# Optimization experiments

Measured on AMD Instinct MI355X. Metric: run time of the kernel, lower is better.

## Reference

```python
import jax, jax.numpy as jnp
import numpy as np

B, R, N, D, H = 32, 5, 1024, 256, 256

def setup_inputs() -> dict:
    key = jax.random.key(0)
    k1, k2, k3, k4 = jax.random.split(key, 4)
    nodes = jax.random.normal(k1, (B, N, D), dtype=jnp.float32)
    adj = jax.random.uniform(k2, (B, R, N, N), dtype=jnp.float32)
    # kaiming_normal_ approximation: std = sqrt(2 / fan_in)
    std = np.sqrt(2.0 / D).astype(np.float32)
    w_0 = jax.random.normal(k3, (H, D), dtype=jnp.float32) * std
    w_r = jax.random.normal(k4, (R, H, D), dtype=jnp.float32) * std
    return {"nodes": nodes, "adj": adj, "w_0": w_0, "w_r": w_r}

def reference(nodes, adj, w_0, w_r):
    # nodes: (B,N,D), adj: (B,R,N,N), w_0: (H,D), w_r: (R,H,D)
    xw_0 = jnp.einsum('bnd,hd->bnh', nodes, w_0)            # (B,N,H)
    xw_r = jnp.einsum('bnd,rhd->brnh', nodes, w_r)          # (B,R,N,H)
    c_r = jnp.sum(adj, axis=-1, keepdims=True)              # (B,R,N,1)
    c_r = jnp.where(c_r == 0, jnp.ones_like(c_r), c_r)
    out = jnp.sum(xw_r / c_r, axis=1) + xw_0                # (B,N,H)
    # dropout is identity in eval mode
    return out
```

## Files before the change

### kernel.cpp

```cpp
#include <hip/hip_runtime.h>
#include <hip/hip_bf16.h>


#define BB 32
#define RR 5
#define NN 1024
#define DD 256
#define HH 256
#define MM (BB * NN)

typedef __attribute__((ext_vector_type(8))) short short8;
typedef __attribute__((ext_vector_type(4))) float f32x4;

#define GAS(p) ((const __attribute__((address_space(1))) void*)(p))
#define LAS(p) ((__attribute__((address_space(3))) void*)(p))

__device__ __forceinline__ unsigned short f2bf(float f) {
    unsigned int u = __float_as_uint(f);
    unsigned int r = (u + 0x7FFFu + ((u >> 16) & 1u)) >> 16;
    return (unsigned short)r;
}

__global__ void cvt_kernel(const float* __restrict__ in,
                           unsigned short* __restrict__ out, int n) {
    int i = (blockIdx.x * blockDim.x + threadIdx.x) * 4;
    if (i >= n) return;
    float4 v = *reinterpret_cast<const float4*>(in + i);
    ushort4 o;
    o.x = f2bf(v.x); o.y = f2bf(v.y); o.z = f2bf(v.z); o.w = f2bf(v.w);
    *reinterpret_cast<ushort4*>(out + i) = o;
}

__global__ __launch_bounds__(256) void rowsum_kernel(const float* __restrict__ adj,
                                                     float* __restrict__ inv_c) {
    const int wave = blockIdx.x * 4 + (threadIdx.x >> 6);
    const int lane = threadIdx.x & 63;
    const float4* row4 = reinterpret_cast<const float4*>(adj + (size_t)wave * NN);
    float s = 0.f;
#pragma unroll
    for (int i = 0; i < 4; ++i) {
        float4 v = row4[lane + 64 * i];
        s += (v.x + v.y) + (v.z + v.w);
    }
#pragma unroll
    for (int off = 32; off > 0; off >>= 1) s += __shfl_down(s, off, 64);
    if (lane == 0) {
        float c = (s == 0.f) ? 1.f : s;
        inv_c[wave] = 1.f / c;
    }
}

__global__ __launch_bounds__(256) void gemm_kernel(
    const unsigned short* __restrict__ nodesb,
    const unsigned short* __restrict__ wb,
    const float* __restrict__ inv_c,
    float* __restrict__ out) {
    __shared__ unsigned short smem[14336];
    __shared__ float s_inv[RR * 64];

    const int tid  = threadIdx.x;
    const int lane = tid & 63;
    const int wv   = tid >> 6;
    const int row_base = blockIdx.x * 64;
    const int col_base = blockIdx.y * 64;
    const int m    = lane & 15;
    const int quad = lane >> 4;

    const unsigned short* gp[7];
    unsigned short*       lp[7];
#pragma unroll
    for (int j = 0; j < 7; ++j) {
        const int c = wv * 7 + j;
        lp[j] = smem + c * 512;
        if (c < 4) {
            const int u   = c * 64 + lane;
            const int row = u >> 2;
            const int kc  = u & 3;
            gp[j] = nodesb + (size_t)(row_base + row) * DD + kc * 8;
        } else {
            const int u    = (c - 4) * 64 + lane;
            const int col6 = u >> 2;
            const int kc   = u & 3;
            const int set  = col6 >> 6;
            const int col  = col6 & 63;
            gp[j] = wb + (size_t)(set * HH + col_base + col) * DD + kc * 8;
        }
    }

    f32x4 acc[6][4];
#pragma unroll
    for (int s = 0; s < 6; ++s)
#pragma unroll
        for (int t = 0; t < 4; ++t) acc[s][t] = (f32x4){0.f, 0.f, 0.f, 0.f};

    const unsigned short* aL = smem + m * 32 + quad * 8;
    const unsigned short* bL = smem + 2048 + (wv * 16 + m) * 32 + quad * 8;

    for (int kt = 0; kt < 8; ++kt) {
        __syncthreads();
#pragma unroll
        for (int j = 0; j < 7; ++j)
            __builtin_amdgcn_global_load_lds(GAS(gp[j] + kt * 32), LAS(lp[j]), 16, 0, 0);
        __syncthreads();

        short8 afr[4];
#pragma unroll
        for (int t = 0; t < 4; ++t)
            afr[t] = *reinterpret_cast<const short8*>(aL + t * 512);
#pragma unroll
        for (int s = 0; s < 6; ++s) {
            short8 bfr = *reinterpret_cast<const short8*>(bL + s * 2048);
#pragma unroll
            for (int t = 0; t < 4; ++t)
                acc[s][t] = __builtin_amdgcn_mfma_f32_16x16x32_bf16(afr[t], bfr, acc[s][t], 0, 0, 0);
        }
    }

    const int b  = row_base >> 10;
    const int n0 = row_base & (NN - 1);
    __syncthreads();
#pragma unroll
    for (int i = tid; i < RR * 64; i += 256) {
        const int r = i >> 6, nl = i & 63;
        s_inv[i] = inv_c[((size_t)b * RR + r) * NN + n0 + nl];
    }
    __syncthreads();

    const int hcol = col_base + wv * 16 + m;
#pragma unroll
    for (int t = 0; t < 4; ++t) {
#pragma unroll
        for (int i = 0; i < 4; ++i) {
            const int rloc = t * 16 + quad * 4 + i;
            float v = acc[0][t][i];
#pragma unroll
            for (int r = 0; r < RR; ++r)
                v += s_inv[r * 64 + rloc] * acc[r + 1][t][i];
            out[(size_t)(row_base + rloc) * HH + hcol] = v;
        }
    }
}

extern "C" void kernel_launch(void* const* d_in, const int* in_sizes, int n_in,
                              void* d_out, int out_size, void* d_ws, size_t ws_size,
                              hipStream_t stream) {
    const float* nodes = (const float*)d_in[0];
    const float* adj   = (const float*)d_in[1];
    const float* w0    = (const float*)d_in[2];
    const float* wr    = (const float*)d_in[3];
    float* out = (float*)d_out;

    unsigned short* nodesb = (unsigned short*)d_ws;
    unsigned short* wb     = (unsigned short*)((char*)d_ws + (size_t)MM * DD * 2);
    float*          inv_c  = (float*)((char*)d_ws + (size_t)MM * DD * 2 + (size_t)6 * HH * DD * 2);

    const int n_nodes = MM * DD;
    const int n_w0    = HH * DD;
    const int n_wr    = RR * HH * DD;

    cvt_kernel<<<n_nodes / 4 / 256, 256, 0, stream>>>(nodes, nodesb, n_nodes);
    cvt_kernel<<<n_w0 / 4 / 256, 256, 0, stream>>>(w0, wb, n_w0);
    cvt_kernel<<<n_wr / 4 / 256, 256, 0, stream>>>(wr, wb + n_w0, n_wr);

    rowsum_kernel<<<(BB * RR * NN) / 4, 256, 0, stream>>>(adj, inv_c);

    gemm_kernel<<<dim3(MM / 64, HH / 64), 256, 0, stream>>>(nodesb, wb, inv_c, out);
}
```

Before: 906.4 us.

## Fuse conversion and rowsum kernels; double-buffer GEMM LDS loads

Merges the three bf16 conversion launches and the adjacency row-sum into one prep kernel, so there are fewer launches and the conversion traffic overlaps the adj streaming. The GEMM gets a two-stage LDS ring buffer filled by async global-to-LDS loads, synchronised with vmcnt waits and raw barriers, so loads for tile k+2 overlap compute on tile k. This doubles LDS use per block, which may lower occupancy, and relies on hand-written waitcnt accounting being correct.

```diff
diff --git a/kernel.cpp b/kernel.cpp
--- a/kernel.cpp
+++ b/kernel.cpp
@@ -21,20 +21,33 @@
     return (unsigned short)r;
 }
 
-__global__ void cvt_kernel(const float* __restrict__ in,
-                           unsigned short* __restrict__ out, int n) {
-    int i = (blockIdx.x * blockDim.x + threadIdx.x) * 4;
-    if (i >= n) return;
-    float4 v = *reinterpret_cast<const float4*>(in + i);
-    ushort4 o;
-    o.x = f2bf(v.x); o.y = f2bf(v.y); o.z = f2bf(v.z); o.w = f2bf(v.w);
-    *reinterpret_cast<ushort4*>(out + i) = o;
-}
+__global__ __launch_bounds__(256) void prep_kernel(
+    const float* __restrict__ adj, float* __restrict__ inv_c,
+    const float* __restrict__ nodes, unsigned short* __restrict__ nodesb,
+    const float* __restrict__ w0, const float* __restrict__ wr,
+    unsigned short* __restrict__ wb) {
+    const int tid  = threadIdx.x;
+    const int lane = tid & 63;
 
-__global__ __launch_bounds__(256) void rowsum_kernel(const float* __restrict__ adj,
-                                                     float* __restrict__ inv_c) {
-    const int wave = blockIdx.x * 4 + (threadIdx.x >> 6);
-    const int lane = threadIdx.x & 63;
+    const int gid = blockIdx.x * 256 + tid;
+    const int i4  = gid * 4;
+    if (i4 < MM * DD) {
+        float4 v = *reinterpret_cast<const float4*>(nodes + i4);
+        ushort4 o;
+        o.x = f2bf(v.x); o.y = f2bf(v.y); o.z = f2bf(v.z); o.w = f2bf(v.w);
+        *reinterpret_cast<ushort4*>(nodesb + i4) = o;
+    }
+    if (gid < (HH * DD + RR * HH * DD) / 4) {
+        const int i = gid * 4;
+        float4 v;
+        if (i < HH * DD) v = *reinterpret_cast<const float4*>(w0 + i);
+        else             v = *reinterpret_cast<const float4*>(wr + (i - HH * DD));
+        ushort4 o;
+        o.x = f2bf(v.x); o.y = f2bf(v.y); o.z = f2bf(v.z); o.w = f2bf(v.w);
+        *reinterpret_cast<ushort4*>(wb + i) = o;
+    }
+
+    const int wave = blockIdx.x * 4 + (tid >> 6);
     const float4* row4 = reinterpret_cast<const float4*>(adj + (size_t)wave * NN);
     float s = 0.f;
 #pragma unroll
@@ -55,7 +68,7 @@
     const unsigned short* __restrict__ wb,
     const float* __restrict__ inv_c,
     float* __restrict__ out) {
-    __shared__ unsigned short smem[14336];
+    __shared__ unsigned short smem[2 * 14336];
     __shared__ float s_inv[RR * 64];
 
     const int tid  = threadIdx.x;
@@ -93,26 +106,41 @@
 #pragma unroll
         for (int t = 0; t < 4; ++t) acc[s][t] = (f32x4){0.f, 0.f, 0.f, 0.f};
 
-    const unsigned short* aL = smem + m * 32 + quad * 8;
-    const unsigned short* bL = smem + 2048 + (wv * 16 + m) * 32 + quad * 8;
+    const int aoff = m * 32 + quad * 8;
+    const int boff = 2048 + (wv * 16 + m) * 32 + quad * 8;
 
+#pragma unroll
+    for (int j = 0; j < 7; ++j)
+        __builtin_amdgcn_global_load_lds(GAS(gp[j]), LAS(lp[j]), 16, 0, 0);
+#pragma unroll
+    for (int j = 0; j < 7; ++j)
+        __builtin_amdgcn_global_load_lds(GAS(gp[j] + 32), LAS(lp[j] + 14336), 16, 0, 0);
+
+#pragma unroll
     for (int kt = 0; kt < 8; ++kt) {
-        __syncthreads();
-#pragma unroll
-        for (int j = 0; j < 7; ++j)
-            __builtin_amdgcn_global_load_lds(GAS(gp[j] + kt * 32), LAS(lp[j]), 16, 0, 0);
-        __syncthreads();
+        if (kt < 7) asm volatile("s_waitcnt vmcnt(7)" ::: "memory");
+        else        asm volatile("s_waitcnt vmcnt(0)" ::: "memory");
+        asm volatile("s_barrier" ::: "memory");
 
+        const unsigned short* base = smem + (kt & 1) * 14336;
         short8 afr[4];
 #pragma unroll
         for (int t = 0; t < 4; ++t)
-            afr[t] = *reinterpret_cast<const short8*>(aL + t * 512);
+            afr[t] = *reinterpret_cast<const short8*>(base + aoff + t * 512);
 #pragma unroll
         for (int s = 0; s < 6; ++s) {
-            short8 bfr = *reinterpret_cast<const short8*>(bL + s * 2048);
+            short8 bfr = *reinterpret_cast<const short8*>(base + boff + s * 2048);
 #pragma unroll
             for (int t = 0; t < 4; ++t)
                 acc[s][t] = __builtin_amdgcn_mfma_f32_16x16x32_bf16(afr[t], bfr, acc[s][t], 0, 0, 0);
+        }
+
+        asm volatile("s_barrier" ::: "memory");
+        if (kt < 6) {
+#pragma unroll
+            for (int j = 0; j < 7; ++j)
+                __builtin_amdgcn_global_load_lds(GAS(gp[j] + (kt + 2) * 32),
+                                                 LAS(lp[j] + (kt & 1) * 14336), 16, 0, 0);
         }
     }
 
@@ -154,15 +182,7 @@
     unsigned short* wb     = (unsigned short*)((char*)d_ws + (size_t)MM * DD * 2);
     float*          inv_c  = (float*)((char*)d_ws + (size_t)MM * DD * 2 + (size_t)6 * HH * DD * 2);
 
-    const int n_nodes = MM * DD;
-    const int n_w0    = HH * DD;
-    const int n_wr    = RR * HH * DD;
-
-    cvt_kernel<<<n_nodes / 4 / 256, 256, 0, stream>>>(nodes, nodesb, n_nodes);
-    cvt_kernel<<<n_w0 / 4 / 256, 256, 0, stream>>>(w0, wb, n_w0);
-    cvt_kernel<<<n_wr / 4 / 256, 256, 0, stream>>>(wr, wb + n_w0, n_wr);
-
-    rowsum_kernel<<<(BB * RR * NN) / 4, 256, 0, stream>>>(adj, inv_c);
+    prep_kernel<<<(BB * RR * NN) / 4, 256, 0, stream>>>(adj, inv_c, nodes, nodesb, w0, wr, wb);
 
     gemm_kernel<<<dim3(MM / 64, HH / 64), 256, 0, stream>>>(nodesb, wb, inv_c, out);
 }
```

Result: no change. 912.9 us (+0.7%).
